# Kernel tuning notes

Hardware: AMD Instinct MI355X
Metric: run time of the kernel (lower is better)

## Reference

```python
import jax, jax.numpy as jnp
import numpy as np

DIM = 768
HEADS = 12
DIM_HEAD = 64
INNER = HEADS * DIM_HEAD  # 768
B, N = 8, 1024


def layernorm(x, gamma, beta, eps=1e-5):
    mu = jnp.mean(x, axis=-1, keepdims=True)
    var = jnp.var(x, axis=-1, keepdims=True)
    return (x - mu) * jax.lax.rsqrt(var + eps) * gamma + beta


def setup_inputs() -> dict:
    key = jax.random.key(0)
    ks = jax.random.split(key, 12)
    s = lambda fan_in: 1.0 / np.sqrt(fan_in)
    return {
        "x": jax.random.normal(ks[0], (B, N, DIM), dtype=jnp.float32),
        "ln1_g": jnp.ones((DIM,), jnp.float32),
        "ln1_b": jnp.zeros((DIM,), jnp.float32),
        "ln2_g": jnp.ones((DIM,), jnp.float32),
        "ln2_b": jnp.zeros((DIM,), jnp.float32),
        "w_qkv": jax.random.uniform(ks[1], (DIM, 3 * INNER), jnp.float32, -s(DIM), s(DIM)),
        "w_out": jax.random.uniform(ks[2], (INNER, DIM), jnp.float32, -s(INNER), s(INNER)),
        "b_out": jax.random.uniform(ks[3], (DIM,), jnp.float32, -s(INNER), s(INNER)),
        "w_ff1": jax.random.uniform(ks[4], (DIM, 4 * DIM), jnp.float32, -s(DIM), s(DIM)),
        "b_ff1": jax.random.uniform(ks[5], (4 * DIM,), jnp.float32, -s(DIM), s(DIM)),
        "w_ff2": jax.random.uniform(ks[6], (4 * DIM, DIM), jnp.float32, -s(4 * DIM), s(4 * DIM)),
        "b_ff2": jax.random.uniform(ks[7], (DIM,), jnp.float32, -s(4 * DIM), s(4 * DIM)),
    }


def reference(x, ln1_g, ln1_b, ln2_g, ln2_b, w_qkv, w_out, b_out, w_ff1, b_ff1, w_ff2, b_ff2):
    # --- attention sub-block (dropout = identity, eval mode) ---
    residual = x
    h = layernorm(x, ln1_g, ln1_b)
    qkv = h @ w_qkv  # [B, N, 3*INNER]
    q, k, v = jnp.split(qkv, 3, axis=-1)
    # b n (h d) -> b h n d
    reshape = lambda t: t.reshape(B, N, HEADS, DIM_HEAD).transpose(0, 2, 1, 3)
    q, k, v = reshape(q), reshape(k), reshape(v)
    scale = DIM_HEAD ** -0.5
    attn = jnp.einsum('bhnd,bhmd->bhnm', q, k) * scale
    attn = jax.nn.softmax(attn, axis=-1)
    out = jnp.einsum('bhnm,bhmd->bhnd', attn, v)
    out = out.transpose(0, 2, 1, 3).reshape(B, N, INNER)  # b h n d -> b n (h d)
    out = out @ w_out + b_out
    x = residual + out
    # --- FFN sub-block ---
    h2 = layernorm(x, ln2_g, ln2_b)
    ff = jax.nn.gelu(h2 @ w_ff1 + b_ff1, approximate=False) @ w_ff2 + b_ff2
    return x + ff
```

## Files before the change

### kernel.cpp

```cpp
#include <hip/hip_runtime.h>
#include <hip/hip_bf16.h>
#include <math.h>
#include <stdint.h>

#define BATCH 8
#define SEQ   1024
#define DIM   768
#define HEADS 12
#define DHEAD 64
#define TOK   (BATCH*SEQ)
#define INNER 768
#define FFDIM 3072
#define QKVN  2304
#define QKLD  1536

typedef float floatx4 __attribute__((ext_vector_type(4)));
typedef __bf16 bf16x8 __attribute__((ext_vector_type(8)));

__device__ __forceinline__ float b2f(uint16_t u) {
    return __uint_as_float(((uint32_t)u) << 16);
}
__device__ __forceinline__ uint16_t f2b(float f) {
    uint32_t x = __float_as_uint(f);
    x += 0x7fffu + ((x >> 16) & 1u);
    return (uint16_t)(x >> 16);
}
__device__ __forceinline__ uint32_t cvt_pk_bf16(float lo, float hi) {
    uint32_t r;
    asm("v_cvt_pk_bf16_f32 %0, %1, %2" : "=v"(r) : "v"(lo), "v"(hi));
    return r;
}

__device__ __forceinline__ void gload_lds16(const uint16_t* g, uint16_t* l) {
    __builtin_amdgcn_global_load_lds(
        (const __attribute__((address_space(1))) uint32_t*)g,
        (__attribute__((address_space(3))) uint32_t*)l, 16, 0, 0);
}

__global__ __launch_bounds__(256) void transpose_convert(
    const float* __restrict__ in, uint16_t* __restrict__ outT, int R, int C)
{
    __shared__ float tile[32][33];
    int c0 = blockIdx.x * 32, r0 = blockIdx.y * 32;
    int x = threadIdx.x;
    int y = threadIdx.y;
    #pragma unroll
    for (int i = y; i < 32; i += 8)
        tile[i][x] = in[(size_t)(r0 + i) * C + c0 + x];
    __syncthreads();
    #pragma unroll
    for (int i = y; i < 32; i += 8)
        outT[(size_t)(c0 + i) * R + r0 + x] = f2b(tile[x][i]);
}

__global__ __launch_bounds__(64) void ln_naive(
    const float* __restrict__ x, const float* __restrict__ g,
    const float* __restrict__ be, uint16_t* __restrict__ y)
{
    const int lane = threadIdx.x;
    const size_t row = blockIdx.x;
    float v[12];
    float s = 0.f, ss = 0.f;
    #pragma unroll
    for (int j = 0; j < 12; j++) {
        int idx = lane + j * 64;
        float f = x[row * DIM + idx];
        v[j] = f; s += f; ss += f * f;
    }
    #pragma unroll
    for (int off = 32; off > 0; off >>= 1) {
        s  += __shfl_xor(s, off);
        ss += __shfl_xor(ss, off);
    }
    const float mu = s * (1.f / DIM);
    const float var = ss * (1.f / DIM) - mu * mu;
    const float rstd = rsqrtf(var + 1e-5f);
    #pragma unroll
    for (int j = 0; j < 12; j++) {
        int idx = lane + j * 64;
        y[row * DIM + idx] = f2b((v[j] - mu) * rstd * g[idx] + be[idx]);
    }
}

template<bool BIAS, bool GELU, bool RES, bool OUTF, bool VSPLIT>
__global__ __launch_bounds__(256) void gemm_bt(
    const uint16_t* __restrict__ A, const uint16_t* __restrict__ Bt,
    void* C, const float* __restrict__ bias, int bias_off,
    const float* res, int N, int K, int lda, int ldbt, int ldc,
    uint16_t* __restrict__ vt)
{
    __shared__ __align__(16) uint16_t a_tile[128 * 32];
    __shared__ __align__(16) uint16_t b_tile[128 * 32];
    const int tid = threadIdx.x;
    const int wave = tid >> 6, lane = tid & 63;
    const int wr = wave >> 1, wc = wave & 1;
    const int tileM = blockIdx.y * 128, tileN = blockIdx.x * 128;

    floatx4 acc[4][4] = {};

    const int scol = (tid & 3) * 8;
    const int srow = tid >> 2;
    const int lm = lane & 15;
    const int lq = lane >> 4;
    const int kq = lq * 8;

    for (int k0 = 0; k0 < K; k0 += 32) {
        __syncthreads();
        #pragma unroll
        for (int i = 0; i < 2; i++) {
            int row = i * 64 + srow;
            gload_lds16(A  + (size_t)(tileM + row) * lda  + k0 + scol, &a_tile[row * 32 + scol]);
            gload_lds16(Bt + (size_t)(tileN + row) * ldbt + k0 + scol, &b_tile[row * 32 + scol]);
        }
        __syncthreads();

        bf16x8 af[4], bfr[4];
        #pragma unroll
        for (int rt = 0; rt < 4; rt++) {
            int r = wr * 64 + rt * 16 + lm;
            af[rt] = *(const bf16x8*)&a_tile[r * 32 + kq];
        }
        #pragma unroll
        for (int nt = 0; nt < 4; nt++) {
            int n = wc * 64 + nt * 16 + lm;
            bfr[nt] = *(const bf16x8*)&b_tile[n * 32 + kq];
        }
        #pragma unroll
        for (int rt = 0; rt < 4; rt++)
            #pragma unroll
            for (int nt = 0; nt < 4; nt++)
                acc[rt][nt] = __builtin_amdgcn_mfma_f32_16x16x32_bf16(
                    af[rt], bfr[nt], acc[rt][nt], 0, 0, 0);
    }

    const bool vpath = VSPLIT && (tileN >= 1536);
    #pragma unroll
    for (int rt = 0; rt < 4; rt++) {
        int r0 = tileM + wr * 64 + rt * 16 + lq * 4;
        #pragma unroll
        for (int nt = 0; nt < 4; nt++) {
            int cg = tileN + wc * 64 + nt * 16 + lm;
            if (vpath) {
                int d = cg - 1536;
                int bb = r0 >> 10, s0 = r0 & 1023;
                uint32_t p0 = (uint32_t)f2b(acc[rt][nt][0]) | ((uint32_t)f2b(acc[rt][nt][1]) << 16);
                uint32_t p1 = (uint32_t)f2b(acc[rt][nt][2]) | ((uint32_t)f2b(acc[rt][nt][3]) << 16);
                uint2 pk; pk.x = p0; pk.y = p1;
                *(uint2*)&vt[((size_t)bb * 768 + d) * 1024 + s0] = pk;
            } else {
                float bvv = BIAS ? bias[bias_off + cg] : 0.f;
                #pragma unroll
                for (int r = 0; r < 4; r++) {
                    float v = acc[rt][nt][r] + bvv;
                    if (GELU) v = 0.5f * v * (1.f + erff(v * 0.70710678118f));
                    size_t ci = (size_t)(r0 + r) * ldc + cg;
                    if (RES) v += res[ci];
                    if (OUTF) ((float*)C)[ci] = v;
                    else      ((uint16_t*)C)[ci] = f2b(v);
                }
            }
        }
    }
}

#define KSWZ(row, cb) ((cb) ^ (((row) & 7) << 4))
#define NKT (SEQ / 64)

__global__ __launch_bounds__(256) void flash_mfma(
    uint16_t* qk, const uint16_t* __restrict__ vt)
{
    __shared__ __align__(16) uint16_t k_s[64 * 64];
    __shared__ __align__(16) uint16_t v_s[64 * 64];
    __shared__ __align__(16) uint16_t p_s[64 * 64];
    char* k_c = (char*)k_s;
    char* v_c = (char*)v_s;
    char* p_c = (char*)p_s;

    const int t = threadIdx.x;
    const int wq = t >> 6;
    const int lane = t & 63;
    const int lm = lane & 15;
    const int lq = lane >> 4;

    const int qb = blockIdx.x, h = blockIdx.y, b = blockIdx.z;
    const size_t rowbase = (size_t)b * SEQ;
    const int hcol = h * DHEAD;

    bf16x8 qf[2];
    {
        const uint16_t* qp = qk + (rowbase + qb*64 + wq*16 + lm) * QKLD + hcol + lq*8;
        qf[0] = *(const bf16x8*)qp;
        qf[1] = *(const bf16x8*)(qp + 32);
    }

    floatx4 O[4] = {};
    float m_q = -1e30f, l_q = 0.f;

    const int s_row = t >> 2;
    const int s_cb  = (t & 3) * 32;
    const size_t kgbase = (rowbase + s_row) * QKLD + INNER + hcol;
    const size_t vgbase = ((size_t)b * 768 + hcol + s_row) * 1024;

    uint4 kr0, kr1, vr0, vr1;
    {
        const char* kp = (const char*)(qk + kgbase);
        kr0 = *(const uint4*)(kp + s_cb);
        kr1 = *(const uint4*)(kp + s_cb + 16);
        const char* vp = (const char*)(vt + vgbase);
        vr0 = *(const uint4*)(vp + s_cb);
        vr1 = *(const uint4*)(vp + s_cb + 16);
    }

    for (int kt = 0; kt < NKT; ++kt) {
        *(uint4*)&k_c[s_row*128 + KSWZ(s_row, s_cb)]      = kr0;
        *(uint4*)&k_c[s_row*128 + KSWZ(s_row, s_cb + 16)] = kr1;
        *(uint4*)&v_c[s_row*128 + KSWZ(s_row, s_cb)]      = vr0;
        *(uint4*)&v_c[s_row*128 + KSWZ(s_row, s_cb + 16)] = vr1;
        __syncthreads();

        if (kt + 1 < NKT) {
            const char* kp = (const char*)(qk + kgbase + (size_t)(kt + 1) * 64 * QKLD);
            kr0 = *(const uint4*)(kp + s_cb);
            kr1 = *(const uint4*)(kp + s_cb + 16);
            const char* vp = (const char*)(vt + vgbase + (size_t)(kt + 1) * 64);
            vr0 = *(const uint4*)(vp + s_cb);
            vr1 = *(const uint4*)(vp + s_cb + 16);
        }

        floatx4 S[4];
        #pragma unroll
        for (int nt = 0; nt < 4; nt++) {
            const int row = nt*16 + lm;
            bf16x8 ak0 = *(const bf16x8*)&k_c[row*128 + KSWZ(row, lq*16)];
            bf16x8 ak1 = *(const bf16x8*)&k_c[row*128 + KSWZ(row, 64 + lq*16)];
            floatx4 a = {};
            a = __builtin_amdgcn_mfma_f32_16x16x32_bf16(ak0, qf[0], a, 0, 0, 0);
            a = __builtin_amdgcn_mfma_f32_16x16x32_bf16(ak1, qf[1], a, 0, 0, 0);
            S[nt] = a;
        }

        float m0 = fmaxf(fmaxf(S[0][0], S[0][1]), fmaxf(S[0][2], S[0][3]));
        float m1 = fmaxf(fmaxf(S[1][0], S[1][1]), fmaxf(S[1][2], S[1][3]));
        float m2 = fmaxf(fmaxf(S[2][0], S[2][1]), fmaxf(S[2][2], S[2][3]));
        float m3 = fmaxf(fmaxf(S[3][0], S[3][1]), fmaxf(S[3][2], S[3][3]));
        float mx = fmaxf(fmaxf(m0, m1), fmaxf(m2, m3)) * 0.125f;
        mx = fmaxf(mx, __shfl_xor(mx, 16));
        mx = fmaxf(mx, __shfl_xor(mx, 32));
        const float mn = fmaxf(m_q, mx);
        const float alpha = __expf(m_q - mn);
        m_q = mn;

        float p[4][4];
        float sum = 0.f;
        #pragma unroll
        for (int nt = 0; nt < 4; nt++) {
            float p0 = __expf(S[nt][0] * 0.125f - mn);
            float p1 = __expf(S[nt][1] * 0.125f - mn);
            float p2 = __expf(S[nt][2] * 0.125f - mn);
            float p3 = __expf(S[nt][3] * 0.125f - mn);
            p[nt][0] = p0; p[nt][1] = p1; p[nt][2] = p2; p[nt][3] = p3;
            sum += (p0 + p1) + (p2 + p3);
        }
        sum += __shfl_xor(sum, 16);
        sum += __shfl_xor(sum, 32);
        l_q = l_q * alpha + sum;

        const int prow = wq*16 + lm;
        #pragma unroll
        for (int nt = 0; nt < 4; nt++) {
            uint2 w;
            w.x = cvt_pk_bf16(p[nt][0], p[nt][1]);
            w.y = cvt_pk_bf16(p[nt][2], p[nt][3]);
            *(uint2*)&p_c[prow*128 + KSWZ(prow, nt*32 + lq*8)] = w;
        }

        #pragma unroll
        for (int nt = 0; nt < 4; nt++) {
            O[nt][0] *= alpha; O[nt][1] *= alpha;
            O[nt][2] *= alpha; O[nt][3] *= alpha;
        }

        #pragma unroll
        for (int ks = 0; ks < 2; ks++) {
            bf16x8 bp = *(const bf16x8*)&p_c[prow*128 + KSWZ(prow, ks*64 + lq*16)];
            #pragma unroll
            for (int nt = 0; nt < 4; nt++) {
                const int vrow = nt*16 + lm;
                bf16x8 av = *(const bf16x8*)&v_c[vrow*128 + KSWZ(vrow, ks*64 + lq*16)];
                O[nt] = __builtin_amdgcn_mfma_f32_16x16x32_bf16(av, bp, O[nt], 0, 0, 0);
            }
        }
        __syncthreads();
    }

    const float linv = 1.f / l_q;
    uint16_t* dst = qk + (rowbase + qb*64 + wq*16 + lm) * QKLD + hcol;
    #pragma unroll
    for (int nt = 0; nt < 4; nt++) {
        uint2 w;
        w.x = cvt_pk_bf16(O[nt][0] * linv, O[nt][1] * linv);
        w.y = cvt_pk_bf16(O[nt][2] * linv, O[nt][3] * linv);
        *(uint2*)&dst[nt*16 + lq*4] = w;
    }
}

extern "C" void kernel_launch(void* const* d_in, const int* in_sizes, int n_in,
                              void* d_out, int out_size, void* d_ws, size_t ws_size,
                              hipStream_t stream) {
    const float* x      = (const float*)d_in[0];
    const float* ln1_g  = (const float*)d_in[1];
    const float* ln1_b  = (const float*)d_in[2];
    const float* ln2_g  = (const float*)d_in[3];
    const float* ln2_b  = (const float*)d_in[4];
    const float* w_qkv  = (const float*)d_in[5];
    const float* w_out  = (const float*)d_in[6];
    const float* b_out  = (const float*)d_in[7];
    const float* w_ff1  = (const float*)d_in[8];
    const float* b_ff1  = (const float*)d_in[9];
    const float* w_ff2  = (const float*)d_in[10];
    const float* b_ff2  = (const float*)d_in[11];
    float* out = (float*)d_out;

    uint16_t* ws  = (uint16_t*)d_ws;
    uint16_t* qk  = ws;
    uint16_t* ffc = ws;
    uint16_t* vT  = ws + (size_t)12582912;
    uint16_t* h   = ws + (size_t)18874368;
    uint16_t* WqT = ws + (size_t)25165824;
    uint16_t* WoT = ws + (size_t)26935296;
    uint16_t* W1T = ws + (size_t)27525120;
    uint16_t* W2T = ws + (size_t)29884416;

    dim3 tb(32, 8);
    hipLaunchKernelGGL(transpose_convert, dim3(QKVN/32, DIM/32), tb, 0, stream, w_qkv, WqT, DIM, QKVN);
    hipLaunchKernelGGL(transpose_convert, dim3(DIM/32,  DIM/32), tb, 0, stream, w_out, WoT, DIM, DIM);
    hipLaunchKernelGGL(transpose_convert, dim3(FFDIM/32, DIM/32), tb, 0, stream, w_ff1, W1T, DIM, FFDIM);
    hipLaunchKernelGGL(transpose_convert, dim3(DIM/32, FFDIM/32), tb, 0, stream, w_ff2, W2T, FFDIM, DIM);

    hipLaunchKernelGGL(ln_naive, dim3(TOK), dim3(64), 0, stream, x, ln1_g, ln1_b, h);
    hipLaunchKernelGGL((gemm_bt<false, false, false, false, true>), dim3(QKVN/128, TOK/128), dim3(256), 0, stream,
                       h, WqT, qk, nullptr, 0, nullptr, QKVN, DIM, DIM, DIM, QKLD, vT);
    hipLaunchKernelGGL(flash_mfma, dim3(SEQ/64, HEADS, BATCH), dim3(256), 0, stream, qk, vT);
    hipLaunchKernelGGL((gemm_bt<true, false, true, true, false>), dim3(DIM/128, TOK/128), dim3(256), 0, stream,
                       qk, WoT, out, b_out, 0, x, DIM, INNER, QKLD, DIM, DIM, nullptr);
    hipLaunchKernelGGL(ln_naive, dim3(TOK), dim3(64), 0, stream, out, ln2_g, ln2_b, h);
    for (int c = 0; c < 2; c++) {
        hipLaunchKernelGGL((gemm_bt<true, true, false, false, false>), dim3(1536/128, TOK/128), dim3(256), 0, stream,
                           h, W1T + (size_t)c*1536*DIM, ffc, b_ff1, c*1536, nullptr,
                           1536, DIM, DIM, DIM, 1536, nullptr);
        if (c == 0) {
            hipLaunchKernelGGL((gemm_bt<true, false, true, true, false>), dim3(DIM/128, TOK/128), dim3(256), 0, stream,
                               ffc, W2T + (size_t)c*1536, out, b_ff2, 0, out,
                               DIM, 1536, 1536, FFDIM, DIM, nullptr);
        } else {
            hipLaunchKernelGGL((gemm_bt<false, false, true, true, false>), dim3(DIM/128, TOK/128), dim3(256), 0, stream,
                               ffc, W2T + (size_t)c*1536, out, nullptr, 0, out,
                               DIM, 1536, 1536, FFDIM, DIM, nullptr);
        }
    }
}
```

Baseline: 467.2 us.

## Double-buffer GEMM LDS tiles and remap workgroups across XCDs

The bf16 MFMA GEMM now keeps two LDS buffers for the A and B tiles. It issues the next K-slice's global-to-LDS loads before computing on the current slice, with one barrier per iteration instead of two, so load latency can overlap with MFMA work. It also remaps the linear block id so that consecutive tiles are spread over the eight XCDs when the grid size is a multiple of eight, aiming for better L2 locality. This doubles LDS use per block, which may lower occupancy. The loop relies on the barrier alone to wait for the async LDS loads to finish, with no explicit vmcnt wait inside the loop.

```diff
diff --git a/kernel.cpp b/kernel.cpp
--- a/kernel.cpp
+++ b/kernel.cpp
@@ -82,6 +82,14 @@
     }
 }
 
+#define GEMM_STAGE(buf, kk) do {                                                            \
+    _Pragma("unroll")                                                                       \
+    for (int i = 0; i < 2; i++) {                                                           \
+        int row = i * 64 + srow;                                                            \
+        gload_lds16(A  + (size_t)(tileM + row) * lda  + (kk) + scol, &a_tile[buf][row * 32 + scol]); \
+        gload_lds16(Bt + (size_t)(tileN + row) * ldbt + (kk) + scol, &b_tile[buf][row * 32 + scol]); \
+    } } while (0)
+
 template<bool BIAS, bool GELU, bool RES, bool OUTF, bool VSPLIT>
 __global__ __launch_bounds__(256) void gemm_bt(
     const uint16_t* __restrict__ A, const uint16_t* __restrict__ Bt,
@@ -89,12 +97,18 @@
     const float* res, int N, int K, int lda, int ldbt, int ldc,
     uint16_t* __restrict__ vt)
 {
-    __shared__ __align__(16) uint16_t a_tile[128 * 32];
-    __shared__ __align__(16) uint16_t b_tile[128 * 32];
+    __shared__ __align__(16) uint16_t a_tile[2][128 * 32];
+    __shared__ __align__(16) uint16_t b_tile[2][128 * 32];
     const int tid = threadIdx.x;
     const int wave = tid >> 6, lane = tid & 63;
     const int wr = wave >> 1, wc = wave & 1;
-    const int tileM = blockIdx.y * 128, tileN = blockIdx.x * 128;
+
+    const int nwg = gridDim.x * gridDim.y;
+    int bid = blockIdx.y * gridDim.x + blockIdx.x;
+    if ((nwg & 7) == 0)
+        bid = (bid & 7) * (nwg >> 3) + (bid >> 3);
+    const int tileM = (bid / gridDim.x) * 128;
+    const int tileN = (bid % gridDim.x) * 128;
 
     floatx4 acc[4][4] = {};
 
@@ -104,26 +118,24 @@
     const int lq = lane >> 4;
     const int kq = lq * 8;
 
+    GEMM_STAGE(0, 0);
+    asm volatile("s_waitcnt vmcnt(0)" ::: "memory");
+    __syncthreads();
+
+    int cur = 0;
     for (int k0 = 0; k0 < K; k0 += 32) {
-        __syncthreads();
-        #pragma unroll
-        for (int i = 0; i < 2; i++) {
-            int row = i * 64 + srow;
-            gload_lds16(A  + (size_t)(tileM + row) * lda  + k0 + scol, &a_tile[row * 32 + scol]);
-            gload_lds16(Bt + (size_t)(tileN + row) * ldbt + k0 + scol, &b_tile[row * 32 + scol]);
-        }
-        __syncthreads();
+        if (k0 + 32 < K) GEMM_STAGE(cur ^ 1, k0 + 32);
 
         bf16x8 af[4], bfr[4];
         #pragma unroll
         for (int rt = 0; rt < 4; rt++) {
             int r = wr * 64 + rt * 16 + lm;
-            af[rt] = *(const bf16x8*)&a_tile[r * 32 + kq];
+            af[rt] = *(const bf16x8*)&a_tile[cur][r * 32 + kq];
         }
         #pragma unroll
         for (int nt = 0; nt < 4; nt++) {
             int n = wc * 64 + nt * 16 + lm;
-            bfr[nt] = *(const bf16x8*)&b_tile[n * 32 + kq];
+            bfr[nt] = *(const bf16x8*)&b_tile[cur][n * 32 + kq];
         }
         #pragma unroll
         for (int rt = 0; rt < 4; rt++)
@@ -131,6 +143,9 @@
             for (int nt = 0; nt < 4; nt++)
                 acc[rt][nt] = __builtin_amdgcn_mfma_f32_16x16x32_bf16(
                     af[rt], bfr[nt], acc[rt][nt], 0, 0, 0);
+
+        __syncthreads();
+        cur ^= 1;
     }
 
     const bool vpath = VSPLIT && (tileN >= 1536);
```

Measured after the change: 443.9 us. -5.0%, faster.
